# Kernel optimization log

Hardware: AMD Instinct MI355X
Metric: run time of the kernel (lower is better)

Reference implementation:

```python
import jax, jax.numpy as jnp
import numpy as np

B, S, D = 4, 2048, 1024
H = 2 * D          # hidden_dim = 2*n_embd
A = H // 16        # adapt_dim = 128
E = 8              # num_experts
K = 2              # top-k within group
GS = 4             # group_size
G = E // GS        # num_groups


def _ln(x, g, b, eps=1e-5):
    m = x.mean(-1, keepdims=True)
    v = x.var(-1, keepdims=True)
    return (x - m) / jnp.sqrt(v + eps) * g + b


def setup_inputs() -> dict:
    key = jax.random.key(0)
    ks = jax.random.split(key, 12)
    s = 1.0 / np.sqrt(D)       # shared MLP init scale
    sa = s * 0.01              # adapt layers init scale
    se = 0.01 / np.sqrt(A)     # expert adapter init scale
    f32 = jnp.float32
    return {
        "x": jax.random.normal(ks[0], (B, S, D), f32),
        "W_up": jax.random.normal(ks[1], (H, D), f32) * s,
        "W_gate": jax.random.normal(ks[2], (H, D), f32) * s,
        "W_down": jax.random.normal(ks[3], (D, H), f32) * s,
        "W_pre": jax.random.normal(ks[4], (A, D), f32) * sa,
        "W_post": jax.random.normal(ks[5], (A, H), f32) * sa,
        "g_an": jnp.ones((A,), f32),
        "b_an": jnp.zeros((A,), f32),
        "W_aproj": jax.random.normal(ks[6], (H, A), f32) * sa,
        "W_eadapt": jax.random.normal(ks[7], (E, A, A), f32) * se,
        "g_e": jnp.ones((E, A), f32),
        "b_e": jnp.zeros((E, A), f32),
        "W_eproj": jax.random.normal(ks[8], (H, A), f32) * se,
        "W_oproj": jax.random.normal(ks[9], (D, H), f32) * se,
        "W_rg": jax.random.normal(ks[10], (G, D), f32) * 0.001,
        "W_re": jax.random.normal(ks[11], (GS, D), f32) * 0.001,
    }


def reference(x, W_up, W_gate, W_down, W_pre, W_post, g_an, b_an, W_aproj,
              W_eadapt, g_e, b_e, W_eproj, W_oproj, W_rg, W_re):
    Bs, Ss, Ds = x.shape
    N = Bs * Ss
    xf = x.reshape(N, Ds)

    # ---- HierarchicalRouter ----
    gl = xf @ W_rg.T                                   # [N, G]
    gp = jax.nn.softmax(gl, axis=-1)
    gw = gp.max(axis=-1)                               # top-1 group weight
    gi = gp.argmax(axis=-1)                            # top-1 group index
    ll = xf @ W_re.T                                   # [N, GS]
    lp = jax.nn.softmax(ll, axis=-1)
    lw, li = jax.lax.top_k(lp, K)                      # [N, K]
    eidx = gi[:, None] * GS + li                       # global expert ids
    lw = lw / (lw.sum(-1, keepdims=True) + 1e-7)
    fw = gw[:, None] * lw                              # final weights [N, K]
    dispatch = jnp.zeros((N, E), x.dtype).at[jnp.arange(N)[:, None], eidx].set(fw)
    load = dispatch.sum(0)
    target = load.sum() / E
    load_balance_loss = jnp.mean((load - target) ** 2)
    z_loss = jnp.mean(gl ** 2) + jnp.mean(ll ** 2)
    router_loss = 0.001 * (load_balance_loss + z_loss)

    # ---- SharedExpertMLP ----
    up = x @ W_up.T                                    # [B, S, H]
    gate = x @ W_gate.T
    hidden = jax.nn.silu(gate) * up
    pre = x @ W_pre.T                                  # [B, S, A]
    a_in = _ln(pre, g_an, b_an)
    a_out = _ln(hidden @ W_post.T, g_an, b_an)
    aw = jax.nn.silu(jnp.clip(jnp.einsum('bsa,bta->bst', a_in, a_out), -5.0, 5.0))
    adapt = jnp.einsum('bst,bta->bsa', aw, a_in) @ W_aproj.T  # [B, S, H]
    hidden = hidden + 0.1 * adapt
    shared = hidden @ W_down.T                         # [B, S, D]

    # ---- ExpertGroup (vectorized gather/MLP/scatter) ----
    # sum_i w_i * (shared + 0.1*contrib_i) = shared*sum(w) + 0.1*sum_i w_i*contrib_i
    w = dispatch.reshape(Bs, Ss, E)                    # dispatch weights
    he = jnp.einsum('bsa,eca->ebsc', pre, W_eadapt)    # [E, B, S, A]
    he = _ln(he, g_e[:, None, None, :], b_e[:, None, None, :])
    wh = jnp.einsum('ebsa,bse->bsa', he, w)            # weighted combine at adapt_dim
    contrib = (wh @ W_eproj.T) @ W_oproj.T             # [B, S, D]
    out = shared * w.sum(-1, keepdims=True) + 0.1 * contrib
    return out, router_loss
```

## Files before the change

### kernel.cpp

```cpp
#include <hip/hip_runtime.h>
#include <hip/hip_bf16.h>

typedef unsigned short u16;
typedef short bf16x8 __attribute__((ext_vector_type(8)));
typedef float f32x4 __attribute__((ext_vector_type(4)));

#define N_TOK 8192
#define DIM   1024
#define HID   2048
#define ADIM  128
#define SEQ   2048
#define LDP   2304

__device__ __forceinline__ u16 f2bf_bits(float f){
  unsigned u = __float_as_uint(f);
  unsigned r = (u + 0x7fffu + ((u >> 16) & 1u)) >> 16;
  return (u16)r;
}
__device__ __forceinline__ float bf2f(u16 v){ return __uint_as_float((unsigned)v << 16); }
__device__ __forceinline__ float siluf(float x){ return x / (1.f + __expf(-x)); }

__device__ __forceinline__ void gload16(const void* g, void* l){
  __builtin_amdgcn_global_load_lds((const __attribute__((address_space(1))) void*)g,
                                   (__attribute__((address_space(3))) void*)l, 16, 0, 0);
}

#define SB0() __builtin_amdgcn_sched_barrier(0)

__global__ void __launch_bounds__(512, 2)
gemm_gu256(const u16* __restrict__ X, const u16* __restrict__ Wgu,
           const float* __restrict__ sumw, u16* __restrict__ hidP)
{
  extern __shared__ u16 lds[];
  const int tid = threadIdx.x, w = tid >> 6, lane = tid & 63;
  const int wm = w >> 2, wn = w & 3;
  const int xcd = blockIdx.x & 7, lloc = blockIdx.x >> 3;
  const int bm = (xcd >> 1) * 8 + (lloc & 7);
  const int bn = (xcd & 1) * 8 + (lloc >> 3);
  const long brow = (long)bm * 256, bcol = (long)bn * 256;
  const int frow = lane & 15;
  const int fks = ((lane >> 4) * 8) ^ (((lane >> 1) & 3) << 3);
  const int srow = lane >> 2;
  const int sslot = (((lane & 3) ^ ((lane >> 3) & 3)) * 8);

  f32x4 acc[8][4];
  #pragma unroll
  for (int m = 0; m < 8; m++)
    #pragma unroll
    for (int n = 0; n < 4; n++)
      #pragma unroll
      for (int i = 0; i < 4; i++) acc[m][n][i] = 0.f;

  auto stage = [&](const u16* __restrict__ gbase, long row0, int kt, int kh,
                   int p, int regoff) {
    #pragma unroll
    for (int i = 0; i < 2; i++) {
      const int r = (i * 8 + w) * 16 + srow;
      const u16* g = gbase + (row0 + r) * 1024 + kt * 64 + kh * 32 + sslot;
      u16* l = &lds[p * 32768 + regoff + kh * 8192 + (i * 8 + w) * 512];
      gload16(g, l);
    }
  };

#define AFRAG(mf, kss) (*(const bf16x8*)&lds[p*32768 + (kss)*8192 + (wm*128 + (mf)*16 + frow)*32 + fks])
#define BFRAG(nf, kss) (*(const bf16x8*)&lds[p*32768 + 16384 + (kss)*8192 + (wn*64 + (nf)*16 + frow)*32 + fks])

  stage(X, brow, 0, 0, 0, 0);
  stage(Wgu, bcol, 0, 0, 0, 16384);
  stage(X, brow, 0, 1, 0, 0);
  stage(Wgu, bcol, 0, 1, 0, 16384);
  asm volatile("s_waitcnt vmcnt(4)" ::: "memory");
  __builtin_amdgcn_s_barrier();

  for (int kt = 0; kt < 16; ++kt) {
    const int p = kt & 1, pn = p ^ 1;
    const int ktn = (kt < 15) ? kt + 1 : 15;
    bf16x8 b[4], a[4];

    a[0] = AFRAG(0, 0);
    b[0] = BFRAG(0, 0); b[1] = BFRAG(1, 0); b[2] = BFRAG(2, 0); b[3] = BFRAG(3, 0);
    SB0();
    a[1] = AFRAG(1, 0); SB0();
    a[2] = AFRAG(2, 0); SB0();
    a[3] = AFRAG(3, 0);
    stage(X, brow, ktn, 0, pn, 0);
    __builtin_amdgcn_s_barrier();
    asm volatile("s_waitcnt lgkmcnt(3)" ::: "memory"); SB0();
    __builtin_amdgcn_s_setprio(1);
    #pragma unroll
    for (int n = 0; n < 4; n++)
      acc[0][n] = __builtin_amdgcn_mfma_f32_16x16x32_bf16(a[0], b[n], acc[0][n], 0, 0, 0);
    asm volatile("s_waitcnt lgkmcnt(2)" ::: "memory"); SB0();
    #pragma unroll
    for (int n = 0; n < 4; n++)
      acc[1][n] = __builtin_amdgcn_mfma_f32_16x16x32_bf16(a[1], b[n], acc[1][n], 0, 0, 0);
    asm volatile("s_waitcnt lgkmcnt(1)" ::: "memory"); SB0();
    #pragma unroll
    for (int n = 0; n < 4; n++)
      acc[2][n] = __builtin_amdgcn_mfma_f32_16x16x32_bf16(a[2], b[n], acc[2][n], 0, 0, 0);
    asm volatile("s_waitcnt lgkmcnt(0)" ::: "memory"); SB0();
    #pragma unroll
    for (int n = 0; n < 4; n++)
      acc[3][n] = __builtin_amdgcn_mfma_f32_16x16x32_bf16(a[3], b[n], acc[3][n], 0, 0, 0);
    __builtin_amdgcn_s_setprio(0);
    __builtin_amdgcn_s_barrier();

    a[0] = AFRAG(4, 0); SB0();
    a[1] = AFRAG(5, 0); SB0();
    a[2] = AFRAG(6, 0); SB0();
    a[3] = AFRAG(7, 0);
    stage(Wgu, bcol, ktn, 0, pn, 16384);
    __builtin_amdgcn_s_barrier();
    asm volatile("s_waitcnt lgkmcnt(3)" ::: "memory"); SB0();
    __builtin_amdgcn_s_setprio(1);
    #pragma unroll
    for (int n = 0; n < 4; n++)
      acc[4][n] = __builtin_amdgcn_mfma_f32_16x16x32_bf16(a[0], b[n], acc[4][n], 0, 0, 0);
    asm volatile("s_waitcnt lgkmcnt(2)" ::: "memory"); SB0();
    #pragma unroll
    for (int n = 0; n < 4; n++)
      acc[5][n] = __builtin_amdgcn_mfma_f32_16x16x32_bf16(a[1], b[n], acc[5][n], 0, 0, 0);
    asm volatile("s_waitcnt lgkmcnt(1)" ::: "memory"); SB0();
    #pragma unroll
    for (int n = 0; n < 4; n++)
      acc[6][n] = __builtin_amdgcn_mfma_f32_16x16x32_bf16(a[2], b[n], acc[6][n], 0, 0, 0);
    asm volatile("s_waitcnt lgkmcnt(0)" ::: "memory"); SB0();
    #pragma unroll
    for (int n = 0; n < 4; n++)
      acc[7][n] = __builtin_amdgcn_mfma_f32_16x16x32_bf16(a[3], b[n], acc[7][n], 0, 0, 0);
    __builtin_amdgcn_s_setprio(0);
    asm volatile("s_waitcnt vmcnt(4)" ::: "memory");
    __builtin_amdgcn_s_barrier();

    a[0] = AFRAG(0, 1);
    b[0] = BFRAG(0, 1); b[1] = BFRAG(1, 1); b[2] = BFRAG(2, 1); b[3] = BFRAG(3, 1);
    SB0();
    a[1] = AFRAG(1, 1); SB0();
    a[2] = AFRAG(2, 1); SB0();
    a[3] = AFRAG(3, 1);
    stage(X, brow, ktn, 1, pn, 0);
    __builtin_amdgcn_s_barrier();
    asm volatile("s_waitcnt lgkmcnt(3)" ::: "memory"); SB0();
    __builtin_amdgcn_s_setprio(1);
    #pragma unroll
    for (int n = 0; n < 4; n++)
      acc[0][n] = __builtin_amdgcn_mfma_f32_16x16x32_bf16(a[0], b[n], acc[0][n], 0, 0, 0);
    asm volatile("s_waitcnt lgkmcnt(2)" ::: "memory"); SB0();
    #pragma unroll
    for (int n = 0; n < 4; n++)
      acc[1][n] = __builtin_amdgcn_mfma_f32_16x16x32_bf16(a[1], b[n], acc[1][n], 0, 0, 0);
    asm volatile("s_waitcnt lgkmcnt(1)" ::: "memory"); SB0();
    #pragma unroll
    for (int n = 0; n < 4; n++)
      acc[2][n] = __builtin_amdgcn_mfma_f32_16x16x32_bf16(a[2], b[n], acc[2][n], 0, 0, 0);
    asm volatile("s_waitcnt lgkmcnt(0)" ::: "memory"); SB0();
    #pragma unroll
    for (int n = 0; n < 4; n++)
      acc[3][n] = __builtin_amdgcn_mfma_f32_16x16x32_bf16(a[3], b[n], acc[3][n], 0, 0, 0);
    __builtin_amdgcn_s_setprio(0);
    __builtin_amdgcn_s_barrier();

    a[0] = AFRAG(4, 1); SB0();
    a[1] = AFRAG(5, 1); SB0();
    a[2] = AFRAG(6, 1); SB0();
    a[3] = AFRAG(7, 1);
    stage(Wgu, bcol, ktn, 1, pn, 16384);
    __builtin_amdgcn_s_barrier();
    asm volatile("s_waitcnt lgkmcnt(3)" ::: "memory"); SB0();
    __builtin_amdgcn_s_setprio(1);
    #pragma unroll
    for (int n = 0; n < 4; n++)
      acc[4][n] = __builtin_amdgcn_mfma_f32_16x16x32_bf16(a[0], b[n], acc[4][n], 0, 0, 0);
    asm volatile("s_waitcnt lgkmcnt(2)" ::: "memory"); SB0();
    #pragma unroll
    for (int n = 0; n < 4; n++)
      acc[5][n] = __builtin_amdgcn_mfma_f32_16x16x32_bf16(a[1], b[n], acc[5][n], 0, 0, 0);
    asm volatile("s_waitcnt lgkmcnt(1)" ::: "memory"); SB0();
    #pragma unroll
    for (int n = 0; n < 4; n++)
      acc[6][n] = __builtin_amdgcn_mfma_f32_16x16x32_bf16(a[2], b[n], acc[6][n], 0, 0, 0);
    asm volatile("s_waitcnt lgkmcnt(0)" ::: "memory"); SB0();
    #pragma unroll
    for (int n = 0; n < 4; n++)
      acc[7][n] = __builtin_amdgcn_mfma_f32_16x16x32_bf16(a[3], b[n], acc[7][n], 0, 0, 0);
    __builtin_amdgcn_s_setprio(0);
    asm volatile("s_waitcnt vmcnt(4)" ::: "memory");
    __builtin_amdgcn_s_barrier();
  }
#undef AFRAG
#undef BFRAG

  #pragma unroll
  for (int mf = 0; mf < 8; mf++)
    #pragma unroll
    for (int i = 0; i < 4; i++) {
      const long r = brow + wm * 128 + mf * 16 + (lane >> 4) * 4 + i;
      const float sw = sumw[r];
      #pragma unroll
      for (int q = 0; q < 2; q++) {
        const float g = acc[mf][2 * q][i], u = acc[mf][2 * q + 1][i];
        const int hcol = (bn * 8 + wn * 2 + q) * 16 + (lane & 15);
        hidP[r * LDP + hcol] = f2bf_bits(sw * (siluf(g) * u));
      }
    }
}

__device__ __forceinline__ void kloop128(const u16* __restrict__ A, const u16* __restrict__ B,
                                         int lda, int ldb, int K,
                                         u16* lA, u16* lB, f32x4 (&acc)[4][4])
{
  const int tid = threadIdx.x, wave = tid >> 6, lane = tid & 63;
  const int wr = (wave >> 1) * 64, wc = (wave & 1) * 64;
  const int sr = tid >> 2, sks = ((tid & 3) ^ ((tid >> 3) & 3)) * 8;
  const u16* gA = A + (long)sr * lda + sks;
  const u16* gB = B + (long)sr * ldb + sks;
  const long rA = (long)64 * lda, rB = (long)64 * ldb;
  u16* lA0 = &lA[wave * 512]; u16* lA1 = &lA[2048 + wave * 512];
  u16* lB0 = &lB[wave * 512]; u16* lB1 = &lB[2048 + wave * 512];
  const int frow = lane & 15;
  const int fks = ((lane >> 4) * 8) ^ (((lane >> 1) & 3) << 3);

  for (int kt = 0; kt < K; kt += 32) {
    gload16(gA, lA0); gload16(gA + rA, lA1);
    gload16(gB, lB0); gload16(gB + rB, lB1);
    gA += 32; gB += 32;
    asm volatile("s_waitcnt vmcnt(0)" ::: "memory");
    __syncthreads();
    bf16x8 af[4], bfv[4];
    #pragma unroll
    for (int m = 0; m < 4; m++) af[m] = *(const bf16x8*)&lA[(wr + m * 16 + frow) * 32 + fks];
    #pragma unroll
    for (int n = 0; n < 4; n++) bfv[n] = *(const bf16x8*)&lB[(wc + n * 16 + frow) * 32 + fks];
    #pragma unroll
    for (int m = 0; m < 4; m++)
      #pragma unroll
      for (int n = 0; n < 4; n++)
        acc[m][n] = __builtin_amdgcn_mfma_f32_16x16x32_bf16(af[m], bfv[n], acc[m][n], 0, 0, 0);
    __syncthreads();
  }
}

__device__ __forceinline__ void acc_zero(f32x4 (&acc)[4][4]){
  #pragma unroll
  for (int m = 0; m < 4; m++)
    #pragma unroll
    for (int n = 0; n < 4; n++)
      #pragma unroll
      for (int i = 0; i < 4; i++) acc[m][n][i] = 0.f;
}

__global__ void __launch_bounds__(256, 2)
gemm_silu(const u16* __restrict__ Ag, const u16* __restrict__ Bg,
          u16* __restrict__ bout)
{
  __shared__ u16 lA[4096];
  __shared__ u16 lB[4096];
  const int wave = threadIdx.x >> 6, lane = threadIdx.x & 63;
  const long brow = (long)blockIdx.y * 128, bcol = (long)blockIdx.x * 128;
  const u16* A = Ag + (long)blockIdx.z * (SEQ * ADIM) + brow * ADIM;
  const u16* B = Bg + (long)blockIdx.z * (SEQ * ADIM) + bcol * ADIM;
  f32x4 acc[4][4]; acc_zero(acc);
  kloop128(A, B, ADIM, ADIM, ADIM, lA, lB, acc);
  const int wr = (wave >> 1) * 64, wc = (wave & 1) * 64;
  const long r0 = brow + wr + ((lane >> 4) << 2);
  const long c0 = bcol + wc + (lane & 15);
  u16* O = bout + (long)blockIdx.z * ((long)SEQ * SEQ);
  #pragma unroll
  for (int m = 0; m < 4; m++)
    #pragma unroll
    for (int i = 0; i < 4; i++) {
      long r = r0 + m * 16 + i;
      #pragma unroll
      for (int n = 0; n < 4; n++) {
        float v = acc[m][n][i];
        v = fminf(5.f, fmaxf(-5.f, v));
        O[r * SEQ + c0 + n * 16] = f2bf_bits(siluf(v));
      }
    }
}

__global__ void __launch_bounds__(256, 2)
gemm_split_p1(const u16* __restrict__ aw, const u16* __restrict__ a_inT,
              float* __restrict__ part)
{
  __shared__ u16 lA[4096];
  __shared__ u16 lB[4096];
  const int wave = threadIdx.x >> 6, lane = threadIdx.x & 63;
  const int z = blockIdx.z, batch = z >> 2, split = z & 3;
  const long brow = (long)blockIdx.y * 128;
  const u16* A = aw + (long)batch * SEQ * SEQ + brow * SEQ + (long)split * 512;
  const u16* B = a_inT + (long)batch * ADIM * SEQ + (long)split * 512;
  f32x4 acc[4][4]; acc_zero(acc);
  kloop128(A, B, SEQ, SEQ, 512, lA, lB, acc);
  float* po = part + (long)z * (SEQ * ADIM);
  const int wr = (wave >> 1) * 64, wc = (wave & 1) * 64;
  const long rr = brow + wr + ((lane >> 4) << 2);
  const int cc = wc + (lane & 15);
  #pragma unroll
  for (int m = 0; m < 4; m++)
    #pragma unroll
    for (int i = 0; i < 4; i++) {
      long r = rr + m * 16 + i;
      #pragma unroll
      for (int n = 0; n < 4; n++)
        po[r * 128 + cc + n * 16] = acc[m][n][i];
    }
}

__global__ void __launch_bounds__(256, 2)
split_pq(const u16* __restrict__ xb, const u16* __restrict__ Wpreb,
         const u16* __restrict__ WdQ, const u16* __restrict__ WaTb,
         const u16* __restrict__ Wob, const u16* __restrict__ WeTb,
         float* __restrict__ part, float* __restrict__ qpart)
{
  __shared__ u16 lA[4096];
  __shared__ u16 lB[4096];
  const int blk = blockIdx.x;
  const int wave = threadIdx.x >> 6, lane = threadIdx.x & 63;
  f32x4 acc[4][4]; acc_zero(acc);
  const int wr = (wave >> 1) * 64, wc = (wave & 1) * 64;

  if (blk < 256) {
    const int y = blk & 63, z = blk >> 6;
    const long brow = (long)y * 128;
    const u16* A = xb + brow * DIM + (long)z * 256;
    const u16* B = Wpreb + (long)z * 256;
    kloop128(A, B, DIM, DIM, 256, lA, lB, acc);
    float* po = part + (long)z * (N_TOK * ADIM);
    const long rr = brow + wr + ((lane >> 4) << 2);
    const int cc = wc + (lane & 15);
    #pragma unroll
    for (int m = 0; m < 4; m++)
      #pragma unroll
      for (int i = 0; i < 4; i++) {
        long r = rr + m * 16 + i;
        #pragma unroll
        for (int n = 0; n < 4; n++)
          po[r * 128 + cc + n * 16] = acc[m][n][i];
      }
  } else {
    const int q = blk - 256;
    const int y = q & 7, z = q >> 3;
    const int sel = z >> 2, split = z & 3;
    const long brow = (long)y * 128;
    const int lda = sel ? HID : LDP;
    const u16* A = (sel ? Wob : WdQ) + brow * lda + (long)split * 512;
    const u16* B = (sel ? WeTb : WaTb) + (long)split * 512;
    kloop128(A, B, lda, HID, 512, lA, lB, acc);
    float* po = qpart + (long)z * 131072;
    const long rr = brow + wr + ((lane >> 4) << 2);
    const int cc = wc + (lane & 15);
    #pragma unroll
    for (int m = 0; m < 4; m++)
      #pragma unroll
      for (int i = 0; i < 4; i++) {
        long r = rr + m * 16 + i;
        #pragma unroll
        for (int n = 0; n < 4; n++)
          po[r * 128 + cc + n * 16] = acc[m][n][i];
      }
  }
}

__global__ void __launch_bounds__(256, 2)
he_postf(const u16* __restrict__ preb, const u16* __restrict__ Weadb,
         u16* __restrict__ heb, const u16* __restrict__ hidP,
         const u16* __restrict__ Wpostb, float* __restrict__ postfp)
{
  __shared__ u16 lA[4096];
  __shared__ u16 lB[4096];
  const int blk = blockIdx.x;
  const int wave = threadIdx.x >> 6, lane = threadIdx.x & 63;
  f32x4 acc[4][4]; acc_zero(acc);
  const int wr = (wave >> 1) * 64, wc = (wave & 1) * 64;

  if (blk < 512) {
    const int y = blk & 63, e = blk >> 6;
    const long brow = (long)y * 128;
    const u16* A = preb + brow * ADIM;
    const u16* B = Weadb + (long)e * ADIM * ADIM;
    kloop128(A, B, ADIM, ADIM, ADIM, lA, lB, acc);
    u16* O = heb + (long)e * N_TOK * ADIM;
    const long r0 = brow + wr + ((lane >> 4) << 2);
    const long c0 = wc + (lane & 15);
    #pragma unroll
    for (int m = 0; m < 4; m++)
      #pragma unroll
      for (int i = 0; i < 4; i++) {
        long r = r0 + m * 16 + i;
        #pragma unroll
        for (int n = 0; n < 4; n++)
          O[r * ADIM + c0 + n * 16] = f2bf_bits(acc[m][n][i]);
      }
  } else {
    const int q = blk - 512;
    const int y = q & 63, z = q >> 6;
    const long brow = (long)y * 128;
    const u16* A = hidP + brow * LDP + (long)z * 512;
    const u16* B = Wpostb + (long)z * 512;
    kloop128(A, B, LDP, HID, 512, lA, lB, acc);
    float* po = postfp + (long)z * (N_TOK * ADIM);
    const long rr = brow + wr + ((lane >> 4) << 2);
    const int cc = wc + (lane & 15);
    #pragma unroll
    for (int m = 0; m < 4; m++)
      #pragma unroll
      for (int i = 0; i < 4; i++) {
        long r = rr + m * 16 + i;
        #pragma unroll
        for (int n = 0; n < 4; n++)
          po[r * 128 + cc + n * 16] = acc[m][n][i];
      }
  }
}

__global__ void __launch_bounds__(256, 2)
gemm_f32(const u16* __restrict__ Ag, const u16* __restrict__ Bg,
         const float* __restrict__ stats, float* __restrict__ out)
{
  __shared__ u16 lA[4096];
  __shared__ u16 lB[4096];
  const int wave = threadIdx.x >> 6, lane = threadIdx.x & 63;
  const long brow = (long)blockIdx.y * 128, bcol = (long)blockIdx.x * 128;
  f32x4 acc[4][4]; acc_zero(acc);
  kloop128(Ag + brow * LDP, Bg + bcol * LDP, LDP, LDP, LDP, lA, lB, acc);
  const int wr = (wave >> 1) * 64, wc = (wave & 1) * 64;
  const long r0 = brow + wr + ((lane >> 4) << 2);
  const long c0 = bcol + wc + (lane & 15);
  #pragma unroll
  for (int m = 0; m < 4; m++)
    #pragma unroll
    for (int i = 0; i < 4; i++) {
      long r = r0 + m * 16 + i;
      #pragma unroll
      for (int n = 0; n < 4; n++)
        out[r * DIM + c0 + n * 16] = acc[m][n][i];
    }
  if (blockIdx.x == 0 && blockIdx.y == 0 && threadIdx.x == 0) {
    float tot = 0;
    #pragma unroll
    for (int e = 0; e < 8; e++) tot += stats[e];
    float target = tot * 0.125f;
    float lb = 0;
    #pragma unroll
    for (int e = 0; e < 8; e++) { float d = stats[e] - target; lb += d * d; }
    lb *= 0.125f;
    float z = stats[8] * (1.f / (8192.f * 2.f)) + stats[9] * (1.f / (8192.f * 4.f));
    out[(size_t)N_TOK * DIM] = 0.001f * (lb + z);
  }
}

__global__ void __launch_bounds__(256)
prep_all(const float* __restrict__ x, const float* __restrict__ Wrg,
         const float* __restrict__ Wre, float* __restrict__ sumw,
         float* __restrict__ fwv, int* __restrict__ eidxv,
         float* __restrict__ stats, u16* __restrict__ xb,
         const float* __restrict__ Wg, const float* __restrict__ Wu,
         const float* __restrict__ Wd, const float* __restrict__ Wo,
         const float* __restrict__ Wpost, const float* __restrict__ Wpre,
         const float* __restrict__ Wead,
         u16* __restrict__ Wgu, u16* __restrict__ WdQ,
         u16* __restrict__ Wob, u16* __restrict__ Wpostb,
         u16* __restrict__ Wpreb, u16* __restrict__ Weadb,
         const float* __restrict__ Wa, const float* __restrict__ We,
         u16* __restrict__ Ta, u16* __restrict__ Te)
{
  __shared__ float lst[10];
  const int blk = blockIdx.x;
  if (blk < 512) {
    if (threadIdx.x < 10) lst[threadIdx.x] = 0.f;
    __syncthreads();
    const int wave = threadIdx.x >> 6, lane = threadIdx.x & 63;
    const float4* wg0 = (const float4*)Wrg;
    const float4* wg1 = (const float4*)(Wrg + 1024);
    const float4* we0 = (const float4*)Wre;
    const float4* we1 = (const float4*)(Wre + 1024);
    const float4* we2 = (const float4*)(Wre + 2048);
    const float4* we3 = (const float4*)(Wre + 3072);
    for (int t = 0; t < 4; t++) {
      const long n = (long)blk * 16 + wave * 4 + t;
      const float4* xr = (const float4*)(x + n * 1024);
      float d0 = 0, d1 = 0, t0 = 0, t1 = 0, t2 = 0, t3 = 0;
      #pragma unroll
      for (int j = 0; j < 4; j++) {
        int id = j * 64 + lane;
        float4 xv = xr[id];
        ushort4 xc;
        xc.x = f2bf_bits(xv.x); xc.y = f2bf_bits(xv.y);
        xc.z = f2bf_bits(xv.z); xc.w = f2bf_bits(xv.w);
        *(ushort4*)(xb + n * 1024 + id * 4) = xc;
        float4 a;
        a = wg0[id]; d0 += xv.x * a.x + xv.y * a.y + xv.z * a.z + xv.w * a.w;
        a = wg1[id]; d1 += xv.x * a.x + xv.y * a.y + xv.z * a.z + xv.w * a.w;
        a = we0[id]; t0 += xv.x * a.x + xv.y * a.y + xv.z * a.z + xv.w * a.w;
        a = we1[id]; t1 += xv.x * a.x + xv.y * a.y + xv.z * a.z + xv.w * a.w;
        a = we2[id]; t2 += xv.x * a.x + xv.y * a.y + xv.z * a.z + xv.w * a.w;
        a = we3[id]; t3 += xv.x * a.x + xv.y * a.y + xv.z * a.z + xv.w * a.w;
      }
      #pragma unroll
      for (int o = 32; o; o >>= 1) {
        d0 += __shfl_xor(d0, o); d1 += __shfl_xor(d1, o);
        t0 += __shfl_xor(t0, o); t1 += __shfl_xor(t1, o);
        t2 += __shfl_xor(t2, o); t3 += __shfl_xor(t3, o);
      }
      if (lane == 0) {
        float mg = fmaxf(d0, d1);
        float e0 = __expf(d0 - mg), e1 = __expf(d1 - mg);
        float invg = 1.f / (e0 + e1);
        float p0 = e0 * invg, p1 = e1 * invg;
        int gi = (d1 > d0) ? 1 : 0;
        float gw = fmaxf(p0, p1);
        float l[4] = {t0, t1, t2, t3};
        float ml = fmaxf(fmaxf(l[0], l[1]), fmaxf(l[2], l[3]));
        float p[4]; float su = 0;
        #pragma unroll
        for (int i = 0; i < 4; i++) { p[i] = __expf(l[i] - ml); su += p[i]; }
        float isu = 1.f / su;
        #pragma unroll
        for (int i = 0; i < 4; i++) p[i] *= isu;
        int i1 = 0;
        #pragma unroll
        for (int i = 1; i < 4; i++) if (p[i] > p[i1]) i1 = i;
        int i2 = (i1 == 0) ? 1 : 0;
        #pragma unroll
        for (int i = 0; i < 4; i++) if (i != i1 && p[i] > p[i2]) i2 = i;
        float s2 = p[i1] + p[i2];
        float invs = 1.f / (s2 + 1e-7f);
        float f1 = gw * p[i1] * invs, f2 = gw * p[i2] * invs;
        int ea = gi * 4 + i1, eb = gi * 4 + i2;
        sumw[n] = f1 + f2;
        fwv[2 * n] = f1; fwv[2 * n + 1] = f2;
        eidxv[2 * n] = ea; eidxv[2 * n + 1] = eb;
        atomicAdd(&lst[ea], f1);
        atomicAdd(&lst[eb], f2);
        atomicAdd(&lst[8], d0 * d0 + d1 * d1);
        atomicAdd(&lst[9], t0 * t0 + t1 * t1 + t2 * t2 + t3 * t3);
      }
    }
    __syncthreads();
    if (threadIdx.x < 10) atomicAdd(&stats[threadIdx.x], lst[threadIdx.x]);
  } else if (blk < 4864) {
    long i = ((long)(blk - 512) * 256 + threadIdx.x) * 8;
    const float* s; u16* d; long so, doff;
    if (i < 4194304) {
      long rp = i >> 10, c = i & 1023;
      long i32 = rp >> 5, wi = rp & 31;
      s = (wi < 16) ? Wg : Wu;
      so = (i32 * 16 + (wi & 15)) * 1024 + c;
      d = Wgu; doff = i;
    } else if (i < 6291456) {
      long j = i - 4194304;
      long r = j >> 11, c = j & 2047;
      s = Wd; so = j;
      d = WdQ; doff = r * LDP + c;
    } else if (i < 8388608) { s = Wo;    so = i - 6291456; d = Wob;    doff = so; }
    else if (i < 8650752)   { s = Wpost; so = i - 8388608; d = Wpostb; doff = so; }
    else if (i < 8781824)   { s = Wpre;  so = i - 8650752; d = Wpreb;  doff = so; }
    else                    { s = Wead;  so = i - 8781824; d = Weadb;  doff = so; }
    float4 v0 = *(const float4*)(s + so), v1 = *(const float4*)(s + so + 4);
    ushort4 p, q;
    p.x = f2bf_bits(v0.x); p.y = f2bf_bits(v0.y); p.z = f2bf_bits(v0.z); p.w = f2bf_bits(v0.w);
    q.x = f2bf_bits(v1.x); q.y = f2bf_bits(v1.y); q.z = f2bf_bits(v1.z); q.w = f2bf_bits(v1.w);
    *(ushort4*)(d + doff) = p;
    *(ushort4*)(d + doff + 4) = q;
  } else {
    int bid = blk - 4864;
    const float* src = (bid < 1024) ? Wa : We;
    u16* dst = (bid < 1024) ? Ta : Te;
    int idx = (bid & 1023) * 256 + threadIdx.x;
    int c = idx >> 11, r = idx & 2047;
    dst[idx] = f2bf_bits(src[(long)r * 128 + c]);
  }
}

__global__ void __launch_bounds__(256)
ln1_rq(const float* __restrict__ part, const float* __restrict__ qpart,
       const float* __restrict__ g, const float* __restrict__ b,
       u16* __restrict__ a_in, u16* __restrict__ a_inT, u16* __restrict__ preb,
       u16* __restrict__ WdQ)
{
  const int blk = blockIdx.x;
  if (blk < 2048) {
    int wave = threadIdx.x >> 6, lane = threadIdx.x & 63;
    long n = (long)blk * 4 + wave;
    long base = n * 128;
    float x0 = 0.f, x1 = 0.f;
    #pragma unroll
    for (int s = 0; s < 4; s++) {
      x0 += part[(long)s * (N_TOK * ADIM) + base + lane];
      x1 += part[(long)s * (N_TOK * ADIM) + base + 64 + lane];
    }
    float s2 = x0 + x1, q = x0 * x0 + x1 * x1;
    #pragma unroll
    for (int o = 32; o; o >>= 1) { s2 += __shfl_xor(s2, o); q += __shfl_xor(q, o); }
    float m = s2 * (1.f / 128.f);
    float var = q * (1.f / 128.f) - m * m;
    float inv = rsqrtf(var + 1e-5f);
    float y0 = (x0 - m) * inv * g[lane] + b[lane];
    float y1 = (x1 - m) * inv * g[lane + 64] + b[lane + 64];
    a_in[base + lane] = f2bf_bits(y0);
    a_in[base + 64 + lane] = f2bf_bits(y1);
    long bb = n >> 11, ss = n & 2047;
    a_inT[(bb * 128 + lane) * 2048 + ss] = f2bf_bits(y0);
    a_inT[(bb * 128 + lane + 64) * 2048 + ss] = f2bf_bits(y1);
    preb[base + lane] = f2bf_bits(x0);
    preb[base + 64 + lane] = f2bf_bits(x1);
  } else {
    int idx = (blk - 2048) * 256 + threadIdx.x;
    int r = idx >> 8, c = idx & 255;
    const float* p = qpart + ((c < 128) ? 0 : 524288) + (long)r * 128 + (c & 127);
    float a = p[0] + p[131072] + p[262144] + p[393216];
    WdQ[(long)r * LDP + 2048 + c] = f2bf_bits(a);
  }
}

__global__ void __launch_bounds__(256)
lnc_ln2(const u16* __restrict__ heb, const int* __restrict__ eidxv,
        const float* __restrict__ fwv, const float* __restrict__ g_e,
        const float* __restrict__ b_e, u16* __restrict__ hidP,
        const float* __restrict__ postfp, const float* __restrict__ g_an,
        const float* __restrict__ b_an, const float* __restrict__ sumw,
        u16* __restrict__ a_out)
{
  const int blk = blockIdx.x;
  const int wave = threadIdx.x >> 6, lane = threadIdx.x & 63;
  if (blk < 2048) {
    const long n = (long)blk * 4 + wave;
    float o0 = 0.f, o1 = 0.f;
    #pragma unroll
    for (int k = 0; k < 2; k++) {
      const int e = eidxv[2 * n + k];
      const float w = fwv[2 * n + k];
      const u16* row = heb + ((long)e * N_TOK + n) * 128;
      float h0 = bf2f(row[lane]), h1 = bf2f(row[lane + 64]);
      float s = h0 + h1, q = h0 * h0 + h1 * h1;
      #pragma unroll
      for (int o = 32; o; o >>= 1) { s += __shfl_xor(s, o); q += __shfl_xor(q, o); }
      float m = s * (1.f / 128.f);
      float var = q * (1.f / 128.f) - m * m;
      float inv = rsqrtf(var + 1e-5f);
      o0 += w * ((h0 - m) * inv * g_e[e * 128 + lane] + b_e[e * 128 + lane]);
      o1 += w * ((h1 - m) * inv * g_e[e * 128 + lane + 64] + b_e[e * 128 + lane + 64]);
    }
    hidP[n * LDP + 2176 + lane] = f2bf_bits(0.1f * o0);
    hidP[n * LDP + 2176 + 64 + lane] = f2bf_bits(0.1f * o1);
  } else {
    long n = (long)(blk - 2048) * 4 + wave;
    long base = n * 128;
    float x0 = 0.f, x1 = 0.f;
    #pragma unroll
    for (int s = 0; s < 4; s++) {
      x0 += postfp[(long)s * (N_TOK * ADIM) + base + lane];
      x1 += postfp[(long)s * (N_TOK * ADIM) + base + 64 + lane];
    }
    float invw = 1.f / sumw[n]; x0 *= invw; x1 *= invw;
    float s2 = x0 + x1, q = x0 * x0 + x1 * x1;
    #pragma unroll
    for (int o = 32; o; o >>= 1) { s2 += __shfl_xor(s2, o); q += __shfl_xor(q, o); }
    float m = s2 * (1.f / 128.f);
    float var = q * (1.f / 128.f) - m * m;
    float inv = rsqrtf(var + 1e-5f);
    a_out[base + lane] = f2bf_bits((x0 - m) * inv * g_an[lane] + b_an[lane]);
    a_out[base + 64 + lane] = f2bf_bits((x1 - m) * inv * g_an[lane + 64] + b_an[lane + 64]);
  }
}

__global__ void reduce_part_p1(const float* __restrict__ part,
                               const float* __restrict__ sumw, u16* __restrict__ hidP)
{
  int idx = blockIdx.x * 256 + threadIdx.x;
  int n = idx >> 5, c4 = (idx & 31) * 4;
  int batch = n >> 11, r = n & 2047;
  float4 a = {0.f, 0.f, 0.f, 0.f};
  #pragma unroll
  for (int s = 0; s < 4; s++) {
    float4 v = *(const float4*)(part + (((long)(batch * 4 + s) * 2048 + r) << 7) + c4);
    a.x += v.x; a.y += v.y; a.z += v.z; a.w += v.w;
  }
  float rs = 0.1f * sumw[n];
  ushort4 o;
  o.x = f2bf_bits(rs * a.x); o.y = f2bf_bits(rs * a.y);
  o.z = f2bf_bits(rs * a.z); o.w = f2bf_bits(rs * a.w);
  *(ushort4*)(hidP + (long)n * LDP + 2048 + c4) = o;
}

extern "C" void kernel_launch(void* const* d_in, const int* in_sizes, int n_in,
                              void* d_out, int out_size, void* d_ws, size_t ws_size,
                              hipStream_t stream)
{
  (void)in_sizes; (void)n_in; (void)out_size; (void)ws_size;
  const float* x       = (const float*)d_in[0];
  const float* W_up    = (const float*)d_in[1];
  const float* W_gate  = (const float*)d_in[2];
  const float* W_down  = (const float*)d_in[3];
  const float* W_pre   = (const float*)d_in[4];
  const float* W_post  = (const float*)d_in[5];
  const float* g_an    = (const float*)d_in[6];
  const float* b_an    = (const float*)d_in[7];
  const float* W_aproj = (const float*)d_in[8];
  const float* W_ead   = (const float*)d_in[9];
  const float* g_e     = (const float*)d_in[10];
  const float* b_e     = (const float*)d_in[11];
  const float* W_eproj = (const float*)d_in[12];
  const float* W_oproj = (const float*)d_in[13];
  const float* W_rg    = (const float*)d_in[14];
  const float* W_re    = (const float*)d_in[15];
  float* out = (float*)d_out;

  char* base = (char*)d_ws; size_t off = 0;
  auto alloc = [&](size_t bytes) -> void* {
    void* p = base + off; off = (off + bytes + 255) & ~(size_t)255; return p;
  };
  u16*   xb     = (u16*)  alloc((size_t)N_TOK * DIM * 2);
  u16*   Wgu    = (u16*)  alloc((size_t)2 * HID * DIM * 2);
  u16*   WdQ    = (u16*)  alloc((size_t)DIM * LDP * 2);
  u16*   Wob    = (u16*)  alloc((size_t)DIM * HID * 2);
  u16*   Wpostb = (u16*)  alloc((size_t)ADIM * HID * 2);
  u16*   Wpreb  = (u16*)  alloc((size_t)ADIM * DIM * 2);
  u16*   WaTb   = (u16*)  alloc((size_t)ADIM * HID * 2);
  u16*   WeTb   = (u16*)  alloc((size_t)ADIM * HID * 2);
  u16*   Weadb  = (u16*)  alloc((size_t)8 * ADIM * ADIM * 2);
  u16*   hidP   = (u16*)  alloc((size_t)N_TOK * LDP * 2);
  u16*   heb    = (u16*)  alloc((size_t)8 * N_TOK * ADIM * 2);
  float* part   = (float*)heb;
  u16*   preb   = (u16*)  alloc((size_t)N_TOK * ADIM * 2);
  u16*   a_in   = (u16*)  alloc((size_t)N_TOK * ADIM * 2);
  u16*   a_inT  = (u16*)  alloc((size_t)N_TOK * ADIM * 2);
  u16*   a_out  = (u16*)  alloc((size_t)N_TOK * ADIM * 2);
  float* sumw   = (float*)alloc((size_t)N_TOK * 4);
  float* fwv    = (float*)alloc((size_t)N_TOK * 2 * 4);
  int*   eidxv  = (int*)  alloc((size_t)N_TOK * 2 * 4);
  float* stats  = (float*)alloc(64);
  float* postfp = (float*)d_out;
  float* qpart  = (float*)((char*)d_out + 16777216);
  u16*   aw     = (u16*)d_out;

  hipFuncSetAttribute((const void*)gemm_gu256,
                      hipFuncAttributeMaxDynamicSharedMemorySize, 131072);

  hipMemsetAsync(stats, 0, 64, stream);

  prep_all<<<6912, 256, 0, stream>>>(x, W_rg, W_re, sumw, fwv, eidxv, stats, xb,
                                     W_gate, W_up, W_down, W_oproj, W_post, W_pre,
                                     W_ead, Wgu, WdQ, Wob, Wpostb, Wpreb, Weadb,
                                     W_aproj, W_eproj, WaTb, WeTb);

  gemm_gu256<<<512, 512, 131072, stream>>>(xb, Wgu, sumw, hidP);

  split_pq<<<320, 256, 0, stream>>>(xb, Wpreb, WdQ, WaTb, Wob, WeTb, part, qpart);

  ln1_rq<<<3072, 256, 0, stream>>>(part, qpart, g_an, b_an, a_in, a_inT, preb, WdQ);

  he_postf<<<768, 256, 0, stream>>>(preb, Weadb, heb, hidP, Wpostb, postfp);

  lnc_ln2<<<4096, 256, 0, stream>>>(heb, eidxv, fwv, g_e, b_e, hidP,
                                    postfp, g_an, b_an, sumw, a_out);

  gemm_silu<<<dim3(16, 16, 4), 256, 0, stream>>>(a_in, a_out, aw);

  gemm_split_p1<<<dim3(1, 16, 16), 256, 0, stream>>>(aw, a_inT, part);

  reduce_part_p1<<<1024, 256, 0, stream>>>(part, sumw, hidP);

  gemm_f32<<<dim3(8, 64, 1), 256, 0, stream>>>(hidP, WdQ, stats, out);
}
```

Measured before the change: 243.4 us.

## Fuse adapter score, silu, and weighted sum into flash-style kernel

Replaces the three-kernel adapter path (score GEMM writing a BxSxS bf16 matrix, split-K GEMM writing fp32 partials, and a reduction) with one fused kernel. Each block keeps a 32-row query tile in LDS and streams 128-token key tiles with double buffering, computing the clipped silu scores in LDS and accumulating straight into registers. This removes the large intermediate matrix traffic and two launches. The cost is only 256 blocks with large LDS (144KB, one block per CU), the score work done by every block for its own rows, and a serial loop over 16 tiles.

```diff
diff --git a/kernel.cpp b/kernel.cpp
--- a/kernel.cpp
+++ b/kernel.cpp
@@ -249,62 +249,129 @@
       for (int i = 0; i < 4; i++) acc[m][n][i] = 0.f;
 }
 
+#define FA_AIN 0
+#define FA_S   4096
+#define FA_AO  8192
+#define FA_AI  40960
 __global__ void __launch_bounds__(256, 2)
-gemm_silu(const u16* __restrict__ Ag, const u16* __restrict__ Bg,
-          u16* __restrict__ bout)
-{
-  __shared__ u16 lA[4096];
-  __shared__ u16 lB[4096];
-  const int wave = threadIdx.x >> 6, lane = threadIdx.x & 63;
-  const long brow = (long)blockIdx.y * 128, bcol = (long)blockIdx.x * 128;
-  const u16* A = Ag + (long)blockIdx.z * (SEQ * ADIM) + brow * ADIM;
-  const u16* B = Bg + (long)blockIdx.z * (SEQ * ADIM) + bcol * ADIM;
-  f32x4 acc[4][4]; acc_zero(acc);
-  kloop128(A, B, ADIM, ADIM, ADIM, lA, lB, acc);
-  const int wr = (wave >> 1) * 64, wc = (wave & 1) * 64;
-  const long r0 = brow + wr + ((lane >> 4) << 2);
-  const long c0 = bcol + wc + (lane & 15);
-  u16* O = bout + (long)blockIdx.z * ((long)SEQ * SEQ);
+fused_adapt(const u16* __restrict__ a_in, const u16* __restrict__ a_inT,
+            const u16* __restrict__ a_out, const float* __restrict__ sumw,
+            u16* __restrict__ hidP)
+{
+  extern __shared__ u16 lds[];
+  const int tid = threadIdx.x, w = tid >> 6, lane = tid & 63;
+  const int l15 = lane & 15, khi = lane >> 4;
+  const int b = blockIdx.x >> 6, yt = blockIdx.x & 63;
+  const int n0 = yt * 32;
+  const u16* ain_b  = a_in  + (long)b * SEQ * ADIM;
+  const u16* aout_b = a_out + (long)b * SEQ * ADIM;
+  const u16* ainT_b = a_inT + (long)b * ADIM * SEQ;
+
   #pragma unroll
-  for (int m = 0; m < 4; m++)
-    #pragma unroll
-    for (int i = 0; i < 4; i++) {
-      long r = r0 + m * 16 + i;
-      #pragma unroll
-      for (int n = 0; n < 4; n++) {
-        float v = acc[m][n][i];
-        v = fminf(5.f, fmaxf(-5.f, v));
-        O[r * SEQ + c0 + n * 16] = f2bf_bits(siluf(v));
+  for (int k = 0; k < 2; k++) {
+    int c = tid + k * 256;
+    int row = c >> 4, slot = c & 15;
+    gload16(ain_b + (long)(n0 + row) * ADIM + ((slot ^ (row & 7)) * 8),
+            &lds[FA_AIN + c * 8]);
+  }
+  auto stage_tile = [&](int t0, int pb) {
+    #pragma unroll
+    for (int k = 0; k < 8; k++) {
+      int c = tid + k * 256;
+      int row = c >> 4, slot = c & 15;
+      gload16(aout_b + (long)(t0 + row) * ADIM + ((slot ^ (row & 7)) * 8),
+              &lds[FA_AO + pb * 16384 + c * 8]);
+    }
+    #pragma unroll
+    for (int k = 0; k < 8; k++) {
+      int c = tid + k * 256;
+      int row = c >> 4, slot = c & 15;
+      gload16(ainT_b + (long)row * SEQ + t0 + ((slot ^ (row & 7)) * 8),
+              &lds[FA_AI + pb * 16384 + c * 8]);
+    }
+  };
+  stage_tile(0, 0);
+
+  f32x4 pacc[2][2];
+  #pragma unroll
+  for (int mr = 0; mr < 2; mr++)
+    #pragma unroll
+    for (int nc = 0; nc < 2; nc++)
+      #pragma unroll
+      for (int i = 0; i < 4; i++) pacc[mr][nc][i] = 0.f;
+
+#define LF(base, row, kc) (*(const bf16x8*)&lds[(base) + (row)*128 + (((kc) ^ ((row)&7)) * 8)])
+#define MF(a_, b_, c_) __builtin_amdgcn_mfma_f32_16x16x32_bf16(a_, b_, c_, 0, 0, 0)
+
+  for (int tt = 0; tt < 16; ++tt) {
+    const int p = tt & 1;
+    const int ttn = (tt < 15) ? tt + 1 : 15;
+    stage_tile(ttn * 128, p ^ 1);
+    asm volatile("s_waitcnt vmcnt(16)" ::: "memory");
+    __syncthreads();
+
+    f32x4 sacc[2][2];
+    #pragma unroll
+    for (int mr = 0; mr < 2; mr++)
+      #pragma unroll
+      for (int nc = 0; nc < 2; nc++)
+        #pragma unroll
+        for (int i = 0; i < 4; i++) sacc[mr][nc][i] = 0.f;
+    const int AOb = FA_AO + p * 16384;
+    #pragma unroll
+    for (int ks = 0; ks < 4; ks++) {
+      int kc = ks * 4 + khi;
+      bf16x8 a0 = LF(FA_AIN, l15, kc);
+      bf16x8 a1 = LF(FA_AIN, 16 + l15, kc);
+      bf16x8 b0 = LF(AOb, w * 32 + l15, kc);
+      bf16x8 b1 = LF(AOb, w * 32 + 16 + l15, kc);
+      sacc[0][0] = MF(a0, b0, sacc[0][0]);
+      sacc[0][1] = MF(a0, b1, sacc[0][1]);
+      sacc[1][0] = MF(a1, b0, sacc[1][0]);
+      sacc[1][1] = MF(a1, b1, sacc[1][1]);
+    }
+    #pragma unroll
+    for (int mr = 0; mr < 2; mr++)
+      #pragma unroll
+      for (int nc = 0; nc < 2; nc++)
+        #pragma unroll
+        for (int i = 0; i < 4; i++) {
+          int row = mr * 16 + khi * 4 + i;
+          int col = w * 32 + nc * 16 + l15;
+          float v = fminf(5.f, fmaxf(-5.f, sacc[mr][nc][i]));
+          lds[FA_S + row * 128 + (((col >> 3) ^ (row & 7)) * 8) + (col & 7)] =
+              f2bf_bits(siluf(v));
+        }
+    __syncthreads();
+    const int AIb = FA_AI + p * 16384;
+    #pragma unroll
+    for (int ks = 0; ks < 4; ks++) {
+      int kc = ks * 4 + khi;
+      bf16x8 a0 = LF(FA_S, l15, kc);
+      bf16x8 a1 = LF(FA_S, 16 + l15, kc);
+      bf16x8 b0 = LF(AIb, w * 32 + l15, kc);
+      bf16x8 b1 = LF(AIb, w * 32 + 16 + l15, kc);
+      pacc[0][0] = MF(a0, b0, pacc[0][0]);
+      pacc[0][1] = MF(a0, b1, pacc[0][1]);
+      pacc[1][0] = MF(a1, b0, pacc[1][0]);
+      pacc[1][1] = MF(a1, b1, pacc[1][1]);
+    }
+    __syncthreads();
+  }
+#undef LF
+#undef MF
+
+  const long nb = (long)b * SEQ + n0;
+  #pragma unroll
+  for (int mr = 0; mr < 2; mr++)
+    #pragma unroll
+    for (int nc = 0; nc < 2; nc++)
+      #pragma unroll
+      for (int i = 0; i < 4; i++) {
+        long n = nb + mr * 16 + khi * 4 + i;
+        int c = w * 32 + nc * 16 + l15;
+        hidP[n * LDP + 2048 + c] = f2bf_bits(0.1f * sumw[n] * pacc[mr][nc][i]);
       }
-    }
-}
-
-__global__ void __launch_bounds__(256, 2)
-gemm_split_p1(const u16* __restrict__ aw, const u16* __restrict__ a_inT,
-              float* __restrict__ part)
-{
-  __shared__ u16 lA[4096];
-  __shared__ u16 lB[4096];
-  const int wave = threadIdx.x >> 6, lane = threadIdx.x & 63;
-  const int z = blockIdx.z, batch = z >> 2, split = z & 3;
-  const long brow = (long)blockIdx.y * 128;
-  const u16* A = aw + (long)batch * SEQ * SEQ + brow * SEQ + (long)split * 512;
-  const u16* B = a_inT + (long)batch * ADIM * SEQ + (long)split * 512;
-  f32x4 acc[4][4]; acc_zero(acc);
-  kloop128(A, B, SEQ, SEQ, 512, lA, lB, acc);
-  float* po = part + (long)z * (SEQ * ADIM);
-  const int wr = (wave >> 1) * 64, wc = (wave & 1) * 64;
-  const long rr = brow + wr + ((lane >> 4) << 2);
-  const int cc = wc + (lane & 15);
-  #pragma unroll
-  for (int m = 0; m < 4; m++)
-    #pragma unroll
-    for (int i = 0; i < 4; i++) {
-      long r = rr + m * 16 + i;
-      #pragma unroll
-      for (int n = 0; n < 4; n++)
-        po[r * 128 + cc + n * 16] = acc[m][n][i];
-    }
 }
 
 __global__ void __launch_bounds__(256, 2)
@@ -665,25 +732,6 @@
   }
 }
 
-__global__ void reduce_part_p1(const float* __restrict__ part,
-                               const float* __restrict__ sumw, u16* __restrict__ hidP)
-{
-  int idx = blockIdx.x * 256 + threadIdx.x;
-  int n = idx >> 5, c4 = (idx & 31) * 4;
-  int batch = n >> 11, r = n & 2047;
-  float4 a = {0.f, 0.f, 0.f, 0.f};
-  #pragma unroll
-  for (int s = 0; s < 4; s++) {
-    float4 v = *(const float4*)(part + (((long)(batch * 4 + s) * 2048 + r) << 7) + c4);
-    a.x += v.x; a.y += v.y; a.z += v.z; a.w += v.w;
-  }
-  float rs = 0.1f * sumw[n];
-  ushort4 o;
-  o.x = f2bf_bits(rs * a.x); o.y = f2bf_bits(rs * a.y);
-  o.z = f2bf_bits(rs * a.z); o.w = f2bf_bits(rs * a.w);
-  *(ushort4*)(hidP + (long)n * LDP + 2048 + c4) = o;
-}
-
 extern "C" void kernel_launch(void* const* d_in, const int* in_sizes, int n_in,
                               void* d_out, int out_size, void* d_ws, size_t ws_size,
                               hipStream_t stream)
@@ -733,10 +781,11 @@
   float* stats  = (float*)alloc(64);
   float* postfp = (float*)d_out;
   float* qpart  = (float*)((char*)d_out + 16777216);
-  u16*   aw     = (u16*)d_out;
 
   hipFuncSetAttribute((const void*)gemm_gu256,
                       hipFuncAttributeMaxDynamicSharedMemorySize, 131072);
+  hipFuncSetAttribute((const void*)fused_adapt,
+                      hipFuncAttributeMaxDynamicSharedMemorySize, 147456);
 
   hipMemsetAsync(stats, 0, 64, stream);
 
@@ -756,11 +805,7 @@
   lnc_ln2<<<4096, 256, 0, stream>>>(heb, eidxv, fwv, g_e, b_e, hidP,
                                     postfp, g_an, b_an, sumw, a_out);
 
-  gemm_silu<<<dim3(16, 16, 4), 256, 0, stream>>>(a_in, a_out, aw);
-
-  gemm_split_p1<<<dim3(1, 16, 16), 256, 0, stream>>>(aw, a_inT, part);
-
-  reduce_part_p1<<<1024, 256, 0, stream>>>(part, sumw, hidP);
+  fused_adapt<<<256, 256, 147456, stream>>>(a_in, a_inT, a_out, sumw, hidP);
 
   gemm_f32<<<dim3(8, 64, 1), 256, 0, stream>>>(hidP, WdQ, stats, out);
 }
```

Result: no change. 244.9 us (+0.6%).
